# Optimization experiments

Measured on AMD Instinct MI355X. Metric: run time of the kernel, lower is better.

## Reference

```python
import jax, jax.numpy as jnp
import numpy as np

RADIUS = 2
TOP_K = 8192
TEMPERATURE = 0.1
KSIZE = 2 * RADIUS + 1  # 5


def _hw_grid(dtype):
    # torch: meshgrid(x, x, 'ij') stacked, flattened row-major, cols swapped -> (dx, dy)
    x = jnp.linspace(-RADIUS, RADIUS, KSIZE, dtype=dtype)
    dy, dx = jnp.meshgrid(x, x, indexing='ij')  # dy varies over rows, dx over cols
    return jnp.stack([dx.reshape(-1), dy.reshape(-1)], axis=1)  # (k*k, 2) = (dx, dy)


def _nms2d(x):
    # kornia nms2d: local max pooling (stride 1, SAME padding with -inf), keep only peaks
    r = RADIUS
    xmax = jax.lax.reduce_window(
        x, -jnp.inf, jax.lax.max,
        window_dimensions=(1, 1, KSIZE, KSIZE),
        window_strides=(1, 1, 1, 1),
        padding=((0, 0), (0, 0), (r, r), (r, r)))
    return jnp.where(x == xmax, x, jnp.zeros_like(x))


def _bilinear_sample(img, xy):
    # F.grid_sample(mode='bilinear', align_corners=True) for in-range points.
    # img: (H, W); xy: (N, 2) normalized coords in [-1, 1], (x, y) order.
    H, W = img.shape
    px = (xy[:, 0] + 1.0) * 0.5 * (W - 1)
    py = (xy[:, 1] + 1.0) * 0.5 * (H - 1)
    x0 = jnp.clip(jnp.floor(px).astype(jnp.int32), 0, W - 1)
    y0 = jnp.clip(jnp.floor(py).astype(jnp.int32), 0, H - 1)
    x1 = jnp.clip(x0 + 1, 0, W - 1)
    y1 = jnp.clip(y0 + 1, 0, H - 1)
    wx = px - x0.astype(px.dtype)
    wy = py - y0.astype(py.dtype)
    v00 = img[y0, x0]; v01 = img[y0, x1]
    v10 = img[y1, x0]; v11 = img[y1, x1]
    return (v00 * (1 - wx) * (1 - wy) + v01 * wx * (1 - wy)
            + v10 * (1 - wx) * wy + v11 * wx * wy)


def setup_inputs() -> dict:
    key = jax.random.key(0)
    scores_map = jax.random.uniform(key, (8, 1, 2048, 2048), dtype=jnp.float32)
    return {"scores_map": scores_map}


def reference(scores_map):
    b, _, h, w = scores_map.shape
    r = RADIUS
    dtype = scores_map.dtype

    # --- NMS on detached scores, zero out borders (image_size=None branch) ---
    s_ng = jax.lax.stop_gradient(scores_map)
    nms = _nms2d(s_ng)
    nms = nms.at[:, :, :r, :].set(0.0).at[:, :, :, :r].set(0.0)
    nms = nms.at[:, :, h - r:, :].set(0.0).at[:, :, :, w - r:].set(0.0)

    # --- fixed top-k keypoint selection (top_k > 0 branch) ---
    _, idx = jax.lax.top_k(nms.reshape(b, -1), TOP_K)  # (b, K) flat indices
    ky_i = idx // w
    kx_i = idx % w

    # --- patch extraction == nn.Unfold(kernel, padding=radius) gathered at kpts ---
    padded = jnp.pad(scores_map[:, 0], ((0, 0), (r, r), (r, r)))  # zero pad
    di, dj = jnp.meshgrid(jnp.arange(KSIZE), jnp.arange(KSIZE), indexing='ij')
    di = di.reshape(-1); dj = dj.reshape(-1)  # row-major patch order (matches unfold)
    rows = ky_i[..., None] + di  # (b, K, k*k) ; +r offset absorbed by padding origin
    cols = kx_i[..., None] + dj
    patch = jax.vmap(lambda im, rr, cc: im[rr, cc])(padded, rows, cols)  # (b,K,k2)

    # --- soft-argmax sub-pixel refinement ---
    grid = _hw_grid(dtype)  # (k2, 2) as (dx, dy)
    max_v = jax.lax.stop_gradient(jnp.max(patch, axis=-1, keepdims=True))
    x_exp = jnp.exp((patch - max_v) / TEMPERATURE)       # (b, K, k2)
    x_sum = jnp.sum(x_exp, axis=-1, keepdims=True)       # (b, K, 1)
    xy_res = jnp.einsum('bkp,pc->bkc', x_exp, grid) / x_sum  # (b, K, 2)

    # score dispersity: weighted mean squared distance to the soft centroid
    delta = (grid[None, None, :, :] - xy_res[:, :, None, :]) / r  # (b,K,k2,2)
    dist2 = jnp.sum(delta * delta, axis=-1)                        # (b,K,k2)
    disp = jnp.sum(x_exp * dist2, axis=-1) / jnp.sum(x_exp, axis=-1)  # (b,K)

    # --- normalized keypoint coords and bilinear score resampling ---
    wh = jnp.array([w - 1, h - 1], dtype=dtype)
    kxy = jnp.stack([kx_i.astype(dtype), ky_i.astype(dtype)], axis=-1) + xy_res
    kxy = kxy / wh * 2.0 - 1.0  # (b, K, 2) in [-1, 1]
    kscore = jax.vmap(_bilinear_sample)(scores_map[:, 0], kxy)  # (b, K)

    return kxy, kscore, disp
```

## Files before the change

### kernel.cpp

```cpp
#include <hip/hip_runtime.h>

#define BATCH 8
#define HH 2048
#define WW 2048
#define NPIX (HH*WW)
#define TOPK 8192
#define NB 16384
#define PEAK_CAP 196608
#define CHUNK 32768
#define NCHUNK 6
#define FCHUNK 2048
#define LBINS 2048
#define LO_BIN (NB - LBINS)
#define CAND_CAP 16384

#define OFF_PEAKS  0ull
#define OFF_CANDS  (OFF_PEAKS + (size_t)BATCH*PEAK_CAP*8ull)
#define OFF_HIST   (OFF_CANDS + (size_t)BATCH*CAND_CAP*8ull)
#define OFF_SA     (OFF_HIST  + (size_t)BATCH*NB*4ull)
#define OFF_FILL   (OFF_SA    + (size_t)BATCH*NB*4ull)
#define OFF_PCOUNT (OFF_FILL  + (size_t)BATCH*NB*4ull)
#define OFF_NCAND  (OFF_PCOUNT + 64ull)
#define OFF_BSTAR  (OFF_NCAND + 64ull)
#define OFF_END    (OFF_PCOUNT + 192ull)
#define OFF_PART   (OFF_PCOUNT + 256ull)

__device__ __forceinline__ int bucket_of(float v) {
    int bk = (int)(v * 16384.0f);
    if (bk > NB - 1) bk = NB - 1;
    if (bk < 0) bk = 0;
    return bk;
}

__global__ __launch_bounds__(1024) void k_nms(
    const float* __restrict__ scores,
    unsigned long long* __restrict__ peaks,
    unsigned int* __restrict__ pcount)
{
    const int b = blockIdx.z;
    const int tx = threadIdx.x & 31;
    const int ty = threadIdx.x >> 5;
    const int x = blockIdx.x * 128 + tx * 4;
    const int y = blockIdx.y * 128 + ty * 4;
    const float* img = scores + (size_t)b * NPIX;
    const float4* imgq = (const float4*)img;

    __shared__ unsigned long long lbuf[2048];
    __shared__ unsigned int lcnt;
    __shared__ unsigned int lbase;
    if (threadIdx.x == 0) lcnt = 0;
    __syncthreads();

    const int q = x >> 2;
    const int qm = (q > 0) ? q - 1 : 0;
    const int qp = (q < WW / 4 - 1) ? q + 1 : WW / 4 - 1;

    float hm[8][4];
    float c4[4][4];

#pragma unroll
    for (int j = 0; j < 8; ++j) {
        int gy = y - 2 + j;
        gy = gy < 0 ? 0 : (gy > HH - 1 ? HH - 1 : gy);
        const float4* rowq = imgq + (size_t)gy * (WW / 4);
        const float4 A = rowq[qm];
        const float4 B = rowq[q];
        const float4 C = rowq[qp];
        const float v[12] = {A.x, A.y, A.z, A.w, B.x, B.y, B.z, B.w,
                             C.x, C.y, C.z, C.w};
        float aa[8];
#pragma unroll
        for (int k = 0; k < 8; ++k) aa[k] = fmaxf(v[k + 2], v[k + 3]);
#pragma unroll
        for (int i = 0; i < 4; ++i)
            hm[j][i] = fmaxf(fmaxf(aa[i], aa[i + 2]), v[i + 6]);
        if (j >= 2 && j <= 5) {
#pragma unroll
            for (int i = 0; i < 4; ++i) c4[j - 2][i] = v[i + 4];
        }
    }

#pragma unroll
    for (int r = 0; r < 4; ++r) {
        const int oy = y + r;
        const bool yok = (oy >= 2) && (oy <= HH - 3);
#pragma unroll
        for (int i = 0; i < 4; ++i) {
            const float vm = fmaxf(fmaxf(fmaxf(hm[r][i], hm[r + 1][i]),
                                         fmaxf(hm[r + 2][i], hm[r + 3][i])),
                                   hm[r + 4][i]);
            const float cv = c4[r][i];
            const int col = x + i;
            if (yok && col >= 2 && col <= WW - 3 && cv == vm) {
                unsigned int pos = atomicAdd(&lcnt, 1u);
                if (pos < 2048u) {
                    unsigned int idx = (unsigned int)(oy * WW + col);
                    lbuf[pos] = ((unsigned long long)__float_as_uint(cv) << 32) |
                                (unsigned long long)(~idx);
                }
            }
        }
    }
    __syncthreads();

    unsigned int cnt = lcnt;
    if (cnt > 2048u) cnt = 2048u;
    if (threadIdx.x == 0) lbase = atomicAdd(&pcount[b], cnt);
    __syncthreads();
    const unsigned int gbase = lbase;
    for (unsigned int s = threadIdx.x; s < cnt; s += 1024) {
        unsigned int gpos = gbase + s;
        if (gpos < PEAK_CAP) peaks[(size_t)b * PEAK_CAP + gpos] = lbuf[s];
    }
}

__global__ __launch_bounds__(1024) void k_hist(
    const unsigned long long* __restrict__ peaks,
    const unsigned int* __restrict__ pcount,
    unsigned int* __restrict__ partials)
{
    const int b = blockIdx.y;
    const int blk = blockIdx.x;
    unsigned int n = pcount[b];
    if (n > PEAK_CAP) n = PEAK_CAP;
    const unsigned int base = blk * CHUNK;
    if (base >= n) return;

    __shared__ unsigned int h[NB / 2];
    for (int w = threadIdx.x; w < NB / 2; w += 1024) h[w] = 0u;
    __syncthreads();

    const unsigned int end = (base + CHUNK < n) ? base + CHUNK : n;
    for (unsigned int i = base + threadIdx.x; i < end; i += 1024) {
        unsigned long long key = peaks[(size_t)b * PEAK_CAP + i];
        float v = __uint_as_float((unsigned int)(key >> 32));
        int bk = bucket_of(v);
        atomicAdd(&h[bk >> 1], (bk & 1) ? 0x10000u : 1u);
    }
    __syncthreads();

    unsigned int* dst = partials + ((size_t)(b * NCHUNK + blk)) * (NB / 2);
    for (int w = threadIdx.x; w < NB / 2; w += 1024) dst[w] = h[w];
}

__global__ __launch_bounds__(256) void k_merge(
    const unsigned int* __restrict__ partials,
    const unsigned int* __restrict__ pcount,
    unsigned int* __restrict__ hist)
{
    const int b = blockIdx.y;
    unsigned int n = pcount[b];
    if (n > PEAK_CAP) n = PEAK_CAP;
    const int nblk = (int)((n + CHUNK - 1) / CHUNK);
    const int w = blockIdx.x * 256 + threadIdx.x;

    unsigned int lo = 0, hi = 0;
    for (int k = 0; k < nblk; ++k) {
        const unsigned int p = partials[((size_t)(b * NCHUNK + k)) * (NB / 2) + w];
        lo += p & 0xFFFFu;
        hi += p >> 16;
    }
    ((uint2*)(hist + (size_t)b * NB))[w] = make_uint2(lo, hi);
}

__global__ __launch_bounds__(256) void k_scan(
    const unsigned int* __restrict__ hist,
    unsigned int* __restrict__ SA,
    unsigned int* __restrict__ ncand,
    unsigned int* __restrict__ bstar)
{
    const int b = blockIdx.x;
    unsigned int* sab = SA + b * NB;
    const int t = threadIdx.x;

    __shared__ unsigned int h[NB / 2];
    __shared__ unsigned int ps[256];
    __shared__ int bmax;

    const uint2* hb = (const uint2*)(hist + (size_t)b * NB);
    for (int w = t; w < NB / 2; w += 256) {
        const uint2 p = hb[w];
        h[w] = p.x | (p.y << 16);
    }
    __syncthreads();

    unsigned int sum = 0;
    for (int kk = 0; kk < 32; ++kk) {
        const int k = (kk + t) & 31;
        const unsigned int p = h[t * 32 + k];
        sum += (p & 0xFFFFu) + (p >> 16);
    }
    ps[t] = sum;
    __syncthreads();
    for (int off = 1; off < 256; off <<= 1) {
        unsigned int v = (t + off < 256) ? ps[t + off] : 0u;
        __syncthreads();
        ps[t] += v;
        __syncthreads();
    }
    const unsigned int run0 = ps[t] - sum;

    unsigned int run = run0;
    int bst_local = -1;
    for (int i = 63; i >= 0; --i) {
        const unsigned int w = h[t * 32 + (i >> 1)];
        const unsigned int hv = (i & 1) ? (w >> 16) : (w & 0xFFFFu);
        if (run + hv >= TOPK && bst_local < 0) bst_local = t * 64 + i;
        run += hv;
    }
    if (t == 0) bmax = -1;
    __syncthreads();
    if (bst_local >= 0) atomicMax(&bmax, bst_local);
    __syncthreads();
    const int Bs = bmax < 0 ? 0 : bmax;

    if (t * 64 + 63 >= Bs) {
        run = run0;
        for (int i = 63; i >= 0; --i) {
            const int bin = t * 64 + i;
            const unsigned int w = h[t * 32 + (i >> 1)];
            const unsigned int hv = (i & 1) ? (w >> 16) : (w & 0xFFFFu);
            if (bin >= Bs) sab[bin] = run;
            run += hv;
        }
    }
    __syncthreads();

    if (t == 0) {
        bstar[b] = (unsigned int)Bs;
        const unsigned int w = h[Bs >> 1];
        const unsigned int hv = (Bs & 1) ? (w >> 16) : (w & 0xFFFFu);
        unsigned int nc = sab[Bs] + hv;
        if (nc > CAND_CAP) nc = CAND_CAP;
        ncand[b] = nc;
    }
}

__global__ __launch_bounds__(256) void k_filter(
    const unsigned long long* __restrict__ peaks,
    const unsigned int* __restrict__ pcount,
    const unsigned int* __restrict__ bstar,
    const unsigned int* __restrict__ SA,
    unsigned int* __restrict__ fill,
    unsigned long long* __restrict__ cands)
{
    const int b = blockIdx.y;
    unsigned int n = pcount[b];
    if (n > PEAK_CAP) n = PEAK_CAP;
    const unsigned int base = blockIdx.x * FCHUNK;
    if (base >= n) return;
    const unsigned int end = (base + FCHUNK < n) ? base + FCHUNK : n;
    const unsigned int bs = bstar[b];
    const unsigned long long* pb = peaks + (size_t)b * PEAK_CAP;
    unsigned long long* cb = cands + (size_t)b * CAND_CAP;

    __shared__ unsigned int cnt[LBINS];
    __shared__ unsigned int off[LBINS];
    for (int j = threadIdx.x; j < LBINS; j += 256) { cnt[j] = 0u; off[j] = 0u; }
    __syncthreads();

    for (unsigned int i = base + threadIdx.x; i < end; i += 256) {
        const unsigned long long key = pb[i];
        const float v = __uint_as_float((unsigned int)(key >> 32));
        const int bk = bucket_of(v);
        if ((unsigned int)bk < bs) continue;
        if (bk >= LO_BIN) {
            atomicAdd(&cnt[bk - LO_BIN], 1u);
        } else {
            unsigned int pos = SA[b * NB + bk] + atomicAdd(&fill[b * NB + bk], 1u);
            if (pos < CAND_CAP) cb[pos] = key;
        }
    }
    __syncthreads();

    for (int j = threadIdx.x; j < LBINS; j += 256) {
        const unsigned int c = cnt[j];
        if (c) cnt[j] = atomicAdd(&fill[b * NB + LO_BIN + j], c);
    }
    __syncthreads();

    for (unsigned int i = base + threadIdx.x; i < end; i += 256) {
        const unsigned long long key = pb[i];
        const float v = __uint_as_float((unsigned int)(key >> 32));
        const int bk = bucket_of(v);
        if ((unsigned int)bk < bs || bk < LO_BIN) continue;
        const unsigned int l = atomicAdd(&off[bk - LO_BIN], 1u);
        const unsigned int pos = SA[b * NB + bk] + cnt[bk - LO_BIN] + l;
        if (pos < CAND_CAP) cb[pos] = key;
    }
}

__global__ __launch_bounds__(256) void k_out(
    const float* __restrict__ scores,
    const unsigned long long* __restrict__ cands,
    const unsigned int* __restrict__ ncand,
    const unsigned int* __restrict__ SA,
    const unsigned int* __restrict__ hist,
    float* __restrict__ out)
{
    const int b = blockIdx.y;
    unsigned int n = ncand[b];
    if (n > CAND_CAP) n = CAND_CAP;
    const int base = blockIdx.x * 256;
    const unsigned long long* cb = cands + (size_t)b * CAND_CAP;

    __shared__ unsigned long long seg[1024];
    for (int t = threadIdx.x; t < 1024; t += 256) {
        int gi = base - 384 + t;
        unsigned long long v = 0ull;
        if (gi >= 0 && gi < (int)n) v = cb[gi];
        seg[t] = v;
    }
    __syncthreads();

    unsigned int ci = base + threadIdx.x;
    if (ci >= n) return;

    const unsigned long long key = cb[ci];
    float v = __uint_as_float((unsigned int)(key >> 32));
    const int bk = bucket_of(v);
    const unsigned int seg0 = SA[b * NB + bk];
    const unsigned int len = hist[b * NB + bk];

    unsigned int r = 0;
    if ((int)seg0 >= base - 384 && (int)(seg0 + len) <= base + 640) {
        const int s0 = (int)seg0 - (base - 384);
        for (unsigned int j = 0; j < len; ++j)
            r += (seg[s0 + j] > key) ? 1u : 0u;
    } else {
#pragma unroll 4
        for (unsigned int j = 0; j < len; ++j)
            r += (cb[seg0 + j] > key) ? 1u : 0u;
    }
    const unsigned int rank = seg0 + r;
    if (rank >= TOPK) return;

    const unsigned int idx = ~((unsigned int)(key & 0xFFFFFFFFull));
    const int ky = (int)(idx >> 11);
    const int kx = (int)(idx & (WW - 1));
    const float* img = scores + (size_t)b * NPIX;

    float patch[25];
#pragma unroll
    for (int dy = 0; dy < 5; ++dy) {
#pragma unroll
        for (int dx = 0; dx < 5; ++dx) {
            patch[dy * 5 + dx] = img[(size_t)(ky + dy - 2) * WW + (kx + dx - 2)];
        }
    }
    float mx = patch[0];
#pragma unroll
    for (int p = 1; p < 25; ++p) mx = fmaxf(mx, patch[p]);

    float e[25];
    float s = 0.0f, sx = 0.0f, sy = 0.0f;
#pragma unroll
    for (int p = 0; p < 25; ++p) {
        float ex = expf((patch[p] - mx) * 10.0f);
        e[p] = ex;
        s += ex;
        sx += ex * (float)(p % 5 - 2);
        sy += ex * (float)(p / 5 - 2);
    }
    const float xx = sx / s;
    const float yy = sy / s;

    float dsum = 0.0f;
#pragma unroll
    for (int p = 0; p < 25; ++p) {
        float ddx = ((float)(p % 5 - 2) - xx) * 0.5f;
        float ddy = ((float)(p / 5 - 2) - yy) * 0.5f;
        dsum += e[p] * (ddx * ddx + ddy * ddy);
    }
    const float disp = dsum / s;

    const float kxy_x = ((float)kx + xx) / (float)(WW - 1) * 2.0f - 1.0f;
    const float kxy_y = ((float)ky + yy) / (float)(HH - 1) * 2.0f - 1.0f;

    const float px = (kxy_x + 1.0f) * 0.5f * (float)(WW - 1);
    const float py = (kxy_y + 1.0f) * 0.5f * (float)(HH - 1);
    int x0 = (int)floorf(px); x0 = x0 < 0 ? 0 : (x0 > WW - 1 ? WW - 1 : x0);
    int y0 = (int)floorf(py); y0 = y0 < 0 ? 0 : (y0 > HH - 1 ? HH - 1 : y0);
    int x1 = x0 + 1 > WW - 1 ? WW - 1 : x0 + 1;
    int y1 = y0 + 1 > HH - 1 ? HH - 1 : y0 + 1;
    const float wx = px - (float)x0;
    const float wy = py - (float)y0;
    const float v00 = img[(size_t)y0 * WW + x0];
    const float v01 = img[(size_t)y0 * WW + x1];
    const float v10 = img[(size_t)y1 * WW + x0];
    const float v11 = img[(size_t)y1 * WW + x1];
    const float ksc = v00 * (1.0f - wx) * (1.0f - wy) + v01 * wx * (1.0f - wy)
                    + v10 * (1.0f - wx) * wy + v11 * wx * wy;

    const size_t ok = (size_t)b * TOPK + rank;
    out[2 * ok]     = kxy_x;
    out[2 * ok + 1] = kxy_y;
    out[(size_t)BATCH * TOPK * 2 + ok] = ksc;
    out[(size_t)BATCH * TOPK * 3 + ok] = disp;
}

extern "C" void kernel_launch(void* const* d_in, const int* in_sizes, int n_in,
                              void* d_out, int out_size, void* d_ws, size_t ws_size,
                              hipStream_t stream) {
    const float* scores = (const float*)d_in[0];
    float* out = (float*)d_out;
    char* ws = (char*)d_ws;

    unsigned long long* peaks = (unsigned long long*)(ws + OFF_PEAKS);
    unsigned long long* cands = (unsigned long long*)(ws + OFF_CANDS);
    unsigned int* hist   = (unsigned int*)(ws + OFF_HIST);
    unsigned int* SA     = (unsigned int*)(ws + OFF_SA);
    unsigned int* fill   = (unsigned int*)(ws + OFF_FILL);
    unsigned int* pcount = (unsigned int*)(ws + OFF_PCOUNT);
    unsigned int* ncand  = (unsigned int*)(ws + OFF_NCAND);
    unsigned int* bstar  = (unsigned int*)(ws + OFF_BSTAR);
    unsigned int* part   = (unsigned int*)(ws + OFF_PART);

    hipMemsetAsync(ws + OFF_FILL, 0, (size_t)(OFF_END - OFF_FILL), stream);

    k_nms<<<dim3(WW / 128, HH / 128, BATCH), 1024, 0, stream>>>(scores, peaks, pcount);
    k_hist<<<dim3(NCHUNK, BATCH), 1024, 0, stream>>>(peaks, pcount, part);
    k_merge<<<dim3(NB / 2 / 256, BATCH), 256, 0, stream>>>(part, pcount, hist);
    k_scan<<<dim3(BATCH), 256, 0, stream>>>(hist, SA, ncand, bstar);
    k_filter<<<dim3(PEAK_CAP / FCHUNK, BATCH), 256, 0, stream>>>(peaks, pcount, bstar, SA, fill, cands);
    k_out<<<dim3(CAND_CAP / 256, BATCH), 256, 0, stream>>>(scores, cands, ncand, SA, hist, out);
}
```

Baseline: 277.8 us.

## Fuse histogram merge into scan, shrink memset, buffer top-bin keys in LDS

```diff
diff --git a/kernel.cpp b/kernel.cpp
--- a/kernel.cpp
+++ b/kernel.cpp
@@ -143,33 +143,19 @@
     for (int w = threadIdx.x; w < NB / 2; w += 1024) dst[w] = h[w];
 }
 
-__global__ __launch_bounds__(256) void k_merge(
+__global__ __launch_bounds__(256) void k_scan(
     const unsigned int* __restrict__ partials,
     const unsigned int* __restrict__ pcount,
-    unsigned int* __restrict__ hist)
-{
-    const int b = blockIdx.y;
-    unsigned int n = pcount[b];
-    if (n > PEAK_CAP) n = PEAK_CAP;
-    const int nblk = (int)((n + CHUNK - 1) / CHUNK);
-    const int w = blockIdx.x * 256 + threadIdx.x;
-
-    unsigned int lo = 0, hi = 0;
-    for (int k = 0; k < nblk; ++k) {
-        const unsigned int p = partials[((size_t)(b * NCHUNK + k)) * (NB / 2) + w];
-        lo += p & 0xFFFFu;
-        hi += p >> 16;
-    }
-    ((uint2*)(hist + (size_t)b * NB))[w] = make_uint2(lo, hi);
-}
-
-__global__ __launch_bounds__(256) void k_scan(
-    const unsigned int* __restrict__ hist,
+    unsigned int* __restrict__ hist,
     unsigned int* __restrict__ SA,
+    unsigned int* __restrict__ fill,
     unsigned int* __restrict__ ncand,
     unsigned int* __restrict__ bstar)
 {
     const int b = blockIdx.x;
+    unsigned int n = pcount[b];
+    if (n > PEAK_CAP) n = PEAK_CAP;
+    const int nblk = (int)((n + CHUNK - 1) / CHUNK);
     unsigned int* sab = SA + b * NB;
     const int t = threadIdx.x;
 
@@ -177,10 +163,17 @@
     __shared__ unsigned int ps[256];
     __shared__ int bmax;
 
-    const uint2* hb = (const uint2*)(hist + (size_t)b * NB);
+    for (int w = t; w < NB; w += 256) fill[b * NB + w] = 0u;
+
     for (int w = t; w < NB / 2; w += 256) {
-        const uint2 p = hb[w];
-        h[w] = p.x | (p.y << 16);
+        unsigned int lo = 0, hi = 0;
+        for (int k = 0; k < nblk; ++k) {
+            const unsigned int p = partials[((size_t)(b * NCHUNK + k)) * (NB / 2) + w];
+            lo += p & 0xFFFFu;
+            hi += p >> 16;
+        }
+        h[w] = lo | (hi << 16);
+        ((uint2*)(hist + (size_t)b * NB))[w] = make_uint2(lo, hi);
     }
     __syncthreads();
 
@@ -254,9 +247,12 @@
     const unsigned long long* pb = peaks + (size_t)b * PEAK_CAP;
     unsigned long long* cb = cands + (size_t)b * CAND_CAP;
 
+    __shared__ unsigned long long wbuf[FCHUNK];
     __shared__ unsigned int cnt[LBINS];
     __shared__ unsigned int off[LBINS];
+    __shared__ unsigned int nw;
     for (int j = threadIdx.x; j < LBINS; j += 256) { cnt[j] = 0u; off[j] = 0u; }
+    if (threadIdx.x == 0) nw = 0u;
     __syncthreads();
 
     for (unsigned int i = base + threadIdx.x; i < end; i += 256) {
@@ -265,6 +261,8 @@
         const int bk = bucket_of(v);
         if ((unsigned int)bk < bs) continue;
         if (bk >= LO_BIN) {
+            const unsigned int p = atomicAdd(&nw, 1u);
+            wbuf[p] = key;
             atomicAdd(&cnt[bk - LO_BIN], 1u);
         } else {
             unsigned int pos = SA[b * NB + bk] + atomicAdd(&fill[b * NB + bk], 1u);
@@ -279,11 +277,11 @@
     }
     __syncthreads();
 
-    for (unsigned int i = base + threadIdx.x; i < end; i += 256) {
-        const unsigned long long key = pb[i];
+    const unsigned int w = nw;
+    for (unsigned int i = threadIdx.x; i < w; i += 256) {
+        const unsigned long long key = wbuf[i];
         const float v = __uint_as_float((unsigned int)(key >> 32));
         const int bk = bucket_of(v);
-        if ((unsigned int)bk < bs || bk < LO_BIN) continue;
         const unsigned int l = atomicAdd(&off[bk - LO_BIN], 1u);
         const unsigned int pos = SA[b * NB + bk] + cnt[bk - LO_BIN] + l;
         if (pos < CAND_CAP) cb[pos] = key;
@@ -416,12 +414,11 @@
     unsigned int* bstar  = (unsigned int*)(ws + OFF_BSTAR);
     unsigned int* part   = (unsigned int*)(ws + OFF_PART);
 
-    hipMemsetAsync(ws + OFF_FILL, 0, (size_t)(OFF_END - OFF_FILL), stream);
+    hipMemsetAsync(ws + OFF_PCOUNT, 0, (size_t)(OFF_END - OFF_PCOUNT), stream);
 
     k_nms<<<dim3(WW / 128, HH / 128, BATCH), 1024, 0, stream>>>(scores, peaks, pcount);
     k_hist<<<dim3(NCHUNK, BATCH), 1024, 0, stream>>>(peaks, pcount, part);
-    k_merge<<<dim3(NB / 2 / 256, BATCH), 256, 0, stream>>>(part, pcount, hist);
-    k_scan<<<dim3(BATCH), 256, 0, stream>>>(hist, SA, ncand, bstar);
+    k_scan<<<dim3(BATCH), 256, 0, stream>>>(part, pcount, hist, SA, fill, ncand, bstar);
     k_filter<<<dim3(PEAK_CAP / FCHUNK, BATCH), 256, 0, stream>>>(peaks, pcount, bstar, SA, fill, cands);
     k_out<<<dim3(CAND_CAP / 256, BATCH), 256, 0, stream>>>(scores, cands, ncand, SA, hist, out);
 }
```

After: 318.5 us. 1.15x slower.
